# Kernel tuning notes

Hardware: AMD Instinct MI355X
Metric: run time of the kernel (lower is better)

## Reference

```python
import jax, jax.numpy as jnp
import numpy as np

B, S, D = 8, 2048, 256
H = 2
DK = D // H
DH = 1024  # conv hidden
K = 9
PAD = (K - 1) // 2
EPS = 1e-5


def _layernorm(x, g, b):
    mu = jnp.mean(x, axis=-1, keepdims=True)
    var = jnp.mean(jnp.square(x - mu), axis=-1, keepdims=True)
    return (x - mu) * jax.lax.rsqrt(var + EPS) * g + b


def setup_inputs() -> dict:
    key = jax.random.key(0)
    ks = jax.random.split(key, 12)
    sc = 0.02
    batch = jax.random.normal(ks[0], (B, S, D), dtype=jnp.float32)
    # padding mask: True = past end of sequence
    lengths = jax.random.randint(ks[1], (B,), S // 2, S + 1)
    mask = jnp.arange(S)[None, :] >= lengths[:, None]
    return {
        "batch": batch,
        "mask": mask,
        "wq": jax.random.normal(ks[2], (D, D), jnp.float32) * sc,
        "bq": jnp.zeros((D,), jnp.float32),
        "wk": jax.random.normal(ks[3], (D, D), jnp.float32) * sc,
        "bk": jnp.zeros((D,), jnp.float32),
        "wv": jax.random.normal(ks[4], (D, D), jnp.float32) * sc,
        "bv": jnp.zeros((D,), jnp.float32),
        "wo": jax.random.normal(ks[5], (D, D), jnp.float32) * sc,
        "bo": jnp.zeros((D,), jnp.float32),
        "ln1_g": jnp.ones((D,), jnp.float32),
        "ln1_b": jnp.zeros((D,), jnp.float32),
        "conv1_w": jax.random.normal(ks[6], (DH, D, K), jnp.float32) * sc,
        "conv1_b": jnp.zeros((DH,), jnp.float32),
        "conv2_w": jax.random.normal(ks[7], (D, DH, 1), jnp.float32) * sc,
        "conv2_b": jnp.zeros((D,), jnp.float32),
        "ln2_g": jnp.ones((D,), jnp.float32),
        "ln2_b": jnp.zeros((D,), jnp.float32),
    }


def reference(batch, mask, wq, bq, wk, bk, wv, bv, wo, bo, ln1_g, ln1_b,
              conv1_w, conv1_b, conv2_w, conv2_b, ln2_g, ln2_b):
    b, s, d = batch.shape
    # --- multi-head self-attention ---
    q = (batch @ wq.T + bq).reshape(b, s, H, DK)
    k = (batch @ wk.T + bk).reshape(b, s, H, DK)
    v = (batch @ wv.T + bv).reshape(b, s, H, DK)
    scores = jnp.einsum('bqhd,bkhd->bhqk', q, k) / np.sqrt(d).astype(np.float32)
    scores = jnp.where(mask[:, None, None, :], -jnp.inf, scores)
    attn = jax.nn.softmax(scores, axis=-1)
    ctx = jnp.einsum('bhqk,bkhd->bqhd', attn, v).reshape(b, s, d)
    seq = _layernorm(batch + ctx @ wo.T + bo, ln1_g, ln1_b)
    seq = jnp.where(mask[..., None], 0.0, seq)
    # --- conv FFN ---
    h = jax.lax.conv_general_dilated(
        seq.transpose(0, 2, 1), conv1_w, window_strides=(1,),
        padding=[(PAD, PAD)], dimension_numbers=('NCH', 'OIH', 'NCH'))
    h = jax.nn.relu(h + conv1_b[None, :, None])
    out = jnp.einsum('bhs,oh->bos', h, conv2_w[:, :, 0]) + conv2_b[None, :, None]
    seq = _layernorm(seq + out.transpose(0, 2, 1), ln2_g, ln2_b)
    return jnp.where(mask[..., None], 0.0, seq)
```

## Files before the change

kernel.cpp:

```cpp
#include <hip/hip_runtime.h>

typedef unsigned char  u8;
typedef unsigned short u16;
typedef unsigned int   u32;
typedef __attribute__((ext_vector_type(4))) float f32x4;
typedef __attribute__((ext_vector_type(8))) __bf16 bf16x8;
typedef __attribute__((ext_vector_type(4))) u32  u32x4;
typedef __attribute__((ext_vector_type(2))) u32  u32x2;

__device__ __forceinline__ float bf2f(u16 h){ u32 u = ((u32)h)<<16; return __builtin_bit_cast(float, u); }
__device__ __forceinline__ u16  f2bf(float f){
  u32 u = __builtin_bit_cast(u32, f);
  u32 r = u + 0x7FFFu + ((u>>16)&1u);
  return (u16)(r>>16);
}

typedef const __attribute__((address_space(1))) u32 gas_u32;
typedef __attribute__((address_space(3))) u32 las_u32;
__device__ __forceinline__ void gll16(const void* g, void* l){
  __builtin_amdgcn_global_load_lds((gas_u32*)g, (las_u32*)l, 16, 0, 0);
}

__device__ __forceinline__ f32x4 mfma16(bf16x8 a, bf16x8 b, f32x4 c){
  return __builtin_amdgcn_mfma_f32_16x16x32_bf16(a, b, c, 0, 0, 0);
}

__device__ __forceinline__ bf16x8 ldsr8(const u16* p){
  u32x4 v = *(const u32x4*)p;
  return __builtin_bit_cast(bf16x8, v);
}

__device__ __forceinline__ void xcd_remap(int &m_idx, int &n_idx){
  const int Mt = gridDim.x;
  const int fid = blockIdx.x + Mt*blockIdx.y;
  const int xcd = fid & 7, k = fid >> 3;
  const int mpx = Mt >> 3;
  m_idx = xcd*mpx + (k % mpx);
  n_idx = k / mpx;
}

__global__ __launch_bounds__(256)
void prep_big(const float* __restrict__ batch,
              const float* __restrict__ wq, const float* __restrict__ wk,
              const float* __restrict__ wv, const float* __restrict__ wo,
              const float* __restrict__ w2, const float* __restrict__ w1,
              u16* __restrict__ batchc, u16* __restrict__ wqc, u16* __restrict__ w1r)
{
  const int bid = blockIdx.x, tid = threadIdx.x;
  if (bid < 4096){
    const int i = bid*1024 + tid*4;
    f32x4 v = *(const f32x4*)&batch[i];
    u32x2 o;
    o[0] = (u32)f2bf(v[0]) | ((u32)f2bf(v[1])<<16);
    o[1] = (u32)f2bf(v[2]) | ((u32)f2bf(v[3])<<16);
    *(u32x2*)&batchc[i] = o;
  } else if (bid < 4608){
    const int i = (bid-4096)*1024 + tid*4;
    const float* s; int off;
    if      (i < 65536)  { s = wq; off = i; }
    else if (i < 131072) { s = wk; off = i - 65536; }
    else if (i < 196608) { s = wv; off = i - 131072; }
    else if (i < 262144) { s = wo; off = i - 196608; }
    else                 { s = w2; off = i - 262144; }
    f32x4 v = *(const f32x4*)&s[off];
    u32x2 o;
    o[0] = (u32)f2bf(v[0]) | ((u32)f2bf(v[1])<<16);
    o[1] = (u32)f2bf(v[2]) | ((u32)f2bf(v[3])<<16);
    *(u32x2*)&wqc[i] = o;
  } else {
    const int idx = (bid-4608)*256 + tid;
    const int c = idx / 2304;
    const int t = idx - c*2304;
    const int i = t / 9;
    const int kk = t - i*9;
    w1r[c*2304 + kk*256 + i] = f2bf(w1[idx]);
  }
}

__global__ __launch_bounds__(256)
void prep_small(const float* p0,const float* p1,const float* p2,const float* p3,
                const float* p4,const float* p5,const float* p6,const float* p7,
                const float* p8,const float* p9,
                u16* __restrict__ params, const void* __restrict__ mraw,
                u16* __restrict__ cmask, u32* __restrict__ lengths)
{
  const int bid = blockIdx.x, tid = threadIdx.x;
  if (bid == 0){
    const float* ps[10] = {p0,p1,p2,p3,p4,p5,p6,p7,p8,p9};
    const int  off[10] = {0,256,512,768,1024,1280,1536,1792,2048,3072};
    const int  len[10] = {256,256,256,256,256,256,256,256,1024,256};
    for (int a=0;a<10;++a)
      for (int i=tid;i<len[a];i+=256)
        params[off[a]+i] = f2bf(ps[a][i]);
  } else {
    const u8*  pb8  = (const u8*)mraw;
    const u16* pb16 = (const u16*)mraw;
    const u32* pb32 = (const u32*)mraw;
    __shared__ int bad8, bad16, nz8, nz16;
    __shared__ int slen[8];
    if (tid==0){ bad8=0; bad16=0; nz8=0; nz16=0; }
    if (tid<8) slen[tid] = 2048;
    __syncthreads();
    for (int i=tid;i<16384;i+=256){
      u8 v = pb8[i]; int row = i & 2047;
      if (v>1) atomicOr(&bad8,1);
      if (v){ atomicOr(&nz8,1); if (row<1024) atomicOr(&bad8,1); }
      if (row>0 && pb8[i-1]==1 && v==0) atomicOr(&bad8,1);
    }
    for (int i=tid;i<8192;i+=256){
      u16 v = pb16[i]; int row = i & 2047;
      if (!(v==0 || v==0x3F80)) atomicOr(&bad16,1);
      if (v){ atomicOr(&nz16,1); if (row<1024) atomicOr(&bad16,1); }
      if (row>0 && pb16[i-1]==0x3F80 && v==0) atomicOr(&bad16,1);
    }
    __syncthreads();
    const int mode = (!bad8 && nz8) ? 1 : ((!bad16 && nz16) ? 2 : 0);
    for (int i=tid;i<16384;i+=256){
      u16 m;
      if (mode==1)      m = pb8[i]  ? 1 : 0;
      else if (mode==2) m = pb16[i] ? 1 : 0;
      else              m = pb32[i] ? 1 : 0;
      cmask[i] = m;
      if (m) atomicMin(&slen[i>>11], i&2047);
    }
    __syncthreads();
    if (tid<8) lengths[tid] = (u32)slen[tid];
  }
}

__global__ __launch_bounds__(256)
void zero_halo(u16* __restrict__ seq1p)
{
  const int idx = blockIdx.x*256 + threadIdx.x;
  const int b = idx>>11, t = idx&2047;
  const int r = t>>8, c = t&255;
  const int row = (r<4) ? r : (2052 + r - 4);
  seq1p[((size_t)b*2056 + row)*256 + c] = 0;
}

template<bool ADD_RES>
__global__ __launch_bounds__(256)
void gemm_nt(const u16* __restrict__ A, const u16* __restrict__ W,
             const u16* __restrict__ bias, const u16* __restrict__ res,
             u16* __restrict__ out, int K, const u16* __restrict__ cmask)
{
  __shared__ __align__(16) u16 aL[2][4096];
  __shared__ __align__(16) u16 bL[2][4096];
  const int tid = threadIdx.x, lane = tid&63, w = tid>>6;
  const int wm = w>>1, wn = w&1, lr = lane&15, lg = lane>>4;
  int mi, ni; xcd_remap(mi, ni);
  const int m0 = mi*128, n0 = ni*128;
  if (cmask[m0] != 0) return;
  const int nk = K>>5;

  f32x4 acc[4][4];
#pragma unroll
  for (int i=0;i<4;++i)
#pragma unroll
    for (int j=0;j<4;++j) acc[i][j] = f32x4{0.f,0.f,0.f,0.f};

  auto stage = [&](int buf, int kk){
#pragma unroll
    for (int i=0;i<2;++i){
      const int chunk = w*2+i;
      const int boff  = chunk*1024 + lane*16;
      const int r = boff>>6;
      const int cb = (boff&63) ^ (((r>>1)&3)<<4);
      const int c = cb>>1;
      gll16(&A[(size_t)(m0+r)*K + kk*32 + c], &aL[buf][chunk*512]);
      gll16(&W[(size_t)(n0+r)*K + kk*32 + c], &bL[buf][chunk*512]);
    }
  };

  stage(0,0);
  __syncthreads();
  for (int kk=0; kk<nk; ++kk){
    if (kk+1<nk) stage((kk+1)&1, kk+1);
    const u16* ab = aL[kk&1];
    const u16* bb = bL[kk&1];
    bf16x8 af[4], bv[4];
#pragma unroll
    for (int m=0;m<4;++m){
      const int ra = wm*64+m*16+lr;
      af[m] = ldsr8(&ab[(ra*64 + ((lg*16) ^ (((ra>>1)&3)<<4)))>>1]);
    }
#pragma unroll
    for (int n=0;n<4;++n){
      const int rb = wn*64+n*16+lr;
      bv[n] = ldsr8(&bb[(rb*64 + ((lg*16) ^ (((rb>>1)&3)<<4)))>>1]);
    }
#pragma unroll
    for (int m=0;m<4;++m)
#pragma unroll
      for (int n=0;n<4;++n)
        acc[m][n] = mfma16(af[m], bv[n], acc[m][n]);
    __syncthreads();
  }
#pragma unroll
  for (int m=0;m<4;++m)
#pragma unroll
    for (int n=0;n<4;++n)
#pragma unroll
      for (int r=0;r<4;++r){
        const int row = m0 + wm*64 + m*16 + lg*4 + r;
        const int col = n0 + wn*64 + n*16 + lr;
        float v = acc[m][n][r] + bf2f(bias[col]);
        if constexpr (ADD_RES) v += bf2f(res[(size_t)row*256 + col]);
        out[(size_t)row*256 + col] = f2bf(v);
      }
}

__global__ __launch_bounds__(256)
void gemm_qkv(const u16* __restrict__ A, const u16* __restrict__ W,
              const u16* __restrict__ bias, u16* __restrict__ qbase,
              const u16* __restrict__ cmask)
{
  __shared__ __align__(16) u16 aL[2][4096];
  __shared__ __align__(16) u16 bL[2][4096];
  const int tid = threadIdx.x, lane = tid&63, w = tid>>6;
  const int wm = w>>1, wn = w&1, lr = lane&15, lg = lane>>4;
  int mi, ni; xcd_remap(mi, ni);
  const int m0 = mi*128, n0 = ni*128;
  if (cmask[m0] != 0) return;

  f32x4 acc[4][4];
#pragma unroll
  for (int i=0;i<4;++i)
#pragma unroll
    for (int j=0;j<4;++j) acc[i][j] = f32x4{0.f,0.f,0.f,0.f};

  auto stage = [&](int buf, int kk){
#pragma unroll
    for (int i=0;i<2;++i){
      const int chunk = w*2+i;
      const int boff  = chunk*1024 + lane*16;
      const int r = boff>>6;
      const int cb = (boff&63) ^ (((r>>1)&3)<<4);
      const int c = cb>>1;
      gll16(&A[(size_t)(m0+r)*256 + kk*32 + c], &aL[buf][chunk*512]);
      gll16(&W[(size_t)(n0+r)*256 + kk*32 + c], &bL[buf][chunk*512]);
    }
  };

  stage(0,0);
  __syncthreads();
  for (int kk=0; kk<8; ++kk){
    if (kk+1<8) stage((kk+1)&1, kk+1);
    const u16* ab = aL[kk&1];
    const u16* bb = bL[kk&1];
    bf16x8 af[4], bv[4];
#pragma unroll
    for (int m=0;m<4;++m){
      const int ra = wm*64+m*16+lr;
      af[m] = ldsr8(&ab[(ra*64 + ((lg*16) ^ (((ra>>1)&3)<<4)))>>1]);
    }
#pragma unroll
    for (int n=0;n<4;++n){
      const int rb = wn*64+n*16+lr;
      bv[n] = ldsr8(&bb[(rb*64 + ((lg*16) ^ (((rb>>1)&3)<<4)))>>1]);
    }
#pragma unroll
    for (int m=0;m<4;++m)
#pragma unroll
      for (int n=0;n<4;++n)
        acc[m][n] = mfma16(af[m], bv[n], acc[m][n]);
    __syncthreads();
  }
#pragma unroll
  for (int m=0;m<4;++m)
#pragma unroll
    for (int n=0;n<4;++n)
#pragma unroll
      for (int r=0;r<4;++r){
        const int row = m0 + wm*64 + m*16 + lg*4 + r;
        const int col = n0 + wn*64 + n*16 + lr;
        const int which = col>>8, ch = col&255;
        float v = acc[m][n][r] + bf2f(bias[col]);
        qbase[(size_t)which*4194304 + (size_t)row*256 + ch] = f2bf(v);
      }
}

__global__ __launch_bounds__(256, 4)
void conv1_gemm(const u16* __restrict__ Ap, const u16* __restrict__ W1r,
                const u16* __restrict__ b1, u16* __restrict__ Hout,
                const u16* __restrict__ cmask)
{
  __shared__ __align__(16) u16 aL[2][4096];
  __shared__ __align__(16) u16 bL[2][4096];
  const int tid = threadIdx.x, lane = tid&63, w = tid>>6;
  const int wm = w>>1, wn = w&1, lr = lane&15, lg = lane>>4;
  int mi, ni; xcd_remap(mi, ni);
  const int m0 = mi*128, n0 = ni*128;
  if (cmask[m0] != 0) return;
  const int b = m0>>11, s0 = m0&2047;
  const size_t abase = ((size_t)b*2056 + s0)*256;

  f32x4 acc[4][4];
#pragma unroll
  for (int i=0;i<4;++i)
#pragma unroll
    for (int j=0;j<4;++j) acc[i][j] = f32x4{0.f,0.f,0.f,0.f};

  auto stage = [&](int buf, int kk){
    const int tap = kk>>3, ch0 = (kk&7)*32;
#pragma unroll
    for (int i=0;i<2;++i){
      const int chunk = w*2+i;
      const int boff  = chunk*1024 + lane*16;
      const int r = boff>>6;
      const int cb = (boff&63) ^ (((r>>1)&3)<<4);
      const int c = cb>>1;
      gll16(&Ap[abase + (size_t)(tap + r)*256 + ch0 + c], &aL[buf][chunk*512]);
      gll16(&W1r[(size_t)(n0+r)*2304 + kk*32 + c], &bL[buf][chunk*512]);
    }
  };

  stage(0,0);
  __syncthreads();
  for (int kk=0; kk<72; ++kk){
    if (kk+1<72) stage((kk+1)&1, kk+1);
    const u16* ab = aL[kk&1];
    const u16* bb = bL[kk&1];
    bf16x8 af[4], bv[4];
#pragma unroll
    for (int m=0;m<4;++m){
      const int ra = wm*64+m*16+lr;
      af[m] = ldsr8(&ab[(ra*64 + ((lg*16) ^ (((ra>>1)&3)<<4)))>>1]);
    }
#pragma unroll
    for (int n=0;n<4;++n){
      const int rb = wn*64+n*16+lr;
      bv[n] = ldsr8(&bb[(rb*64 + ((lg*16) ^ (((rb>>1)&3)<<4)))>>1]);
    }
#pragma unroll
    for (int m=0;m<4;++m)
#pragma unroll
      for (int n=0;n<4;++n)
        acc[m][n] = mfma16(af[m], bv[n], acc[m][n]);
    __syncthreads();
  }
#pragma unroll
  for (int m=0;m<4;++m)
#pragma unroll
    for (int n=0;n<4;++n)
#pragma unroll
      for (int r=0;r<4;++r){
        const int row = m0 + wm*64 + m*16 + lg*4 + r;
        const int col = n0 + wn*64 + n*16 + lr;
        float v = acc[m][n][r] + bf2f(b1[col]);
        v = v>0.f ? v : 0.f;
        Hout[(size_t)row*1024 + col] = f2bf(v);
      }
}

__global__ __launch_bounds__(512)
void conv2_ln(const u16* __restrict__ Hh, const u16* __restrict__ w2c,
              const u16* __restrict__ b2, const u16* __restrict__ seq1p,
              const u16* __restrict__ g2, const u16* __restrict__ be2,
              const u16* __restrict__ cmask, float* __restrict__ out)
{
  __shared__ __align__(16) u16 aL[2][2048];
  __shared__ __align__(16) u16 bL[2][8192];
  __shared__ float red[2][32][4][2];
  const int tid = threadIdx.x, lane = tid&63, w = tid>>6;
  const int wm = w>>2, wn = w&3, lr = lane&15, lg = lane>>4;
  int mi, ni; xcd_remap(mi, ni); (void)ni;
  const int m0 = mi*64;
  if (cmask[m0] != 0) return;

  f32x4 acc[2][4];
#pragma unroll
  for (int i=0;i<2;++i)
#pragma unroll
    for (int j=0;j<4;++j) acc[i][j] = f32x4{0.f,0.f,0.f,0.f};

  auto stage = [&](int buf, int kk){
    if (w < 4){
      const int boff = w*1024 + lane*16;
      const int r = boff>>6;
      const int cb = (boff&63) ^ (((r>>1)&3)<<4);
      gll16(&Hh[(size_t)(m0+r)*1024 + kk*32 + (cb>>1)], &aL[buf][w*512]);
    }
#pragma unroll
    for (int i=0;i<2;++i){
      const int chunk = w*2+i;
      const int boff = chunk*1024 + lane*16;
      const int r = boff>>6;
      const int cb = (boff&63) ^ (((r>>1)&3)<<4);
      gll16(&w2c[(size_t)r*1024 + kk*32 + (cb>>1)], &bL[buf][chunk*512]);
    }
  };

  stage(0,0);
  __syncthreads();
  for (int kk=0; kk<32; ++kk){
    if (kk+1<32) stage((kk+1)&1, kk+1);
    const u16* ab = aL[kk&1];
    const u16* bb = bL[kk&1];
    bf16x8 af[2], bv[4];
#pragma unroll
    for (int m=0;m<2;++m){
      const int ra = wm*32+m*16+lr;
      af[m] = ldsr8(&ab[(ra*64 + ((lg*16) ^ (((ra>>1)&3)<<4)))>>1]);
    }
#pragma unroll
    for (int n=0;n<4;++n){
      const int rb = wn*64+n*16+lr;
      bv[n] = ldsr8(&bb[(rb*64 + ((lg*16) ^ (((rb>>1)&3)<<4)))>>1]);
    }
#pragma unroll
    for (int m=0;m<2;++m)
#pragma unroll
      for (int n=0;n<4;++n)
        acc[m][n] = mfma16(af[m], bv[n], acc[m][n]);
    __syncthreads();
  }
#pragma unroll
  for (int m=0;m<2;++m)
#pragma unroll
    for (int r=0;r<4;++r){
      float s = 0.f, qq = 0.f;
#pragma unroll
      for (int n=0;n<4;++n){
        const int col = wn*64 + n*16 + lr;
        const int row = m0 + wm*32 + m*16 + lg*4 + r;
        const size_t ri = ((size_t)row + (row>>11)*8 + 4)*256 + col;
        float val = acc[m][n][r] + bf2f(b2[col]) + bf2f(seq1p[ri]);
        acc[m][n][r] = val;
        s += val; qq += val*val;
      }
#pragma unroll
      for (int x=1;x<16;x<<=1){ s += __shfl_xor(s, x); qq += __shfl_xor(qq, x); }
      if (lr == 0){
        const int lrow = m*16 + lg*4 + r;
        red[wm][lrow][wn][0] = s;
        red[wm][lrow][wn][1] = qq;
      }
    }
  __syncthreads();
#pragma unroll
  for (int m=0;m<2;++m)
#pragma unroll
    for (int r=0;r<4;++r){
      const int lrow = m*16 + lg*4 + r;
      const float S = red[wm][lrow][0][0]+red[wm][lrow][1][0]+red[wm][lrow][2][0]+red[wm][lrow][3][0];
      const float Q = red[wm][lrow][0][1]+red[wm][lrow][1][1]+red[wm][lrow][2][1]+red[wm][lrow][3][1];
      const float mu = S*(1.f/256.f);
      const float rs = rsqrtf(Q*(1.f/256.f) - mu*mu + 1e-5f);
      const int row = m0 + wm*32 + lrow;
      const int msk = cmask[row];
#pragma unroll
      for (int n=0;n<4;++n){
        const int col = wn*64 + n*16 + lr;
        float y = (acc[m][n][r]-mu)*rs*bf2f(g2[col]) + bf2f(be2[col]);
        out[(size_t)row*256 + col] = msk ? 0.f : y;
      }
    }
}

__global__ __launch_bounds__(256)
void vtrans(const u16* __restrict__ V, u16* __restrict__ VT)
{
  __shared__ u16 t[64][72];
  const int tid = threadIdx.x;
  const int s0 = blockIdx.x*64;
  const int d0 = blockIdx.y*64;
#pragma unroll
  for (int i=0;i<2;++i){
    const int chunk = tid + i*256;
    const int sr = chunk>>3, c8 = (chunk&7)*8;
    u32x4 raw = *(const u32x4*)&V[(size_t)(s0+sr)*256 + d0 + c8];
#pragma unroll
    for (int j=0;j<4;++j){
      t[sr][c8+2*j]   = (u16)(raw[j]&0xffffu);
      t[sr][c8+2*j+1] = (u16)(raw[j]>>16);
    }
  }
  __syncthreads();
  const int b = s0>>11;
#pragma unroll
  for (int i=0;i<2;++i){
    const int chunk = tid + i*256;
    const int dr = chunk>>3, s8 = (chunk&7)*8;
    const int dg = d0 + dr;
    const int hh = dg>>7, dh = dg&127;
    u32x4 o;
#pragma unroll
    for (int j=0;j<4;++j)
      o[j] = (u32)t[s8+2*j][dr] | ((u32)t[s8+2*j+1][dr]<<16);
    *(u32x4*)&VT[((size_t)((b*2+hh)*128 + dh))*2048 + (s0&2047) + s8] = o;
  }
}

__global__ __launch_bounds__(512)
void attn_fwd(const u16* __restrict__ Q, const u16* __restrict__ Kb,
              const u16* __restrict__ VT, const u32* __restrict__ lengths,
              u16* __restrict__ ctx)
{
  __shared__ __align__(16) u16 kls[2][64*128];
  __shared__ __align__(16) u16 vtls[2][128*64];
  __shared__ __align__(16) u16 pls[8][16*64];
  const int tid = threadIdx.x, lane = tid&63, w = tid>>6;
  const int fid = blockIdx.x;
  const int pair = fid & 15;
  const int qt = fid >> 4;
  const int b  = pair >> 1;
  const int hh = pair & 1;
  const int q0 = qt*128;
  const int L  = (int)lengths[b];
  if (q0 >= L) return;
  const int nkt = (L + 63) >> 6;
  const int lr = lane&15, lg = lane>>4;
  u16* pw = pls[w];

  bf16x8 qf[4];
#pragma unroll
  for (int d=0;d<4;++d)
    qf[d] = *(const bf16x8*)&Q[((size_t)(b*2048+q0+w*16+lr))*256 + hh*128 + d*32 + lg*8];

  f32x4 oacc[8];
  float mrun[4], lrun[4];
#pragma unroll
  for (int n=0;n<8;++n) oacc[n] = f32x4{0.f,0.f,0.f,0.f};
#pragma unroll
  for (int r=0;r<4;++r){ mrun[r] = -1e30f; lrun[r] = 0.f; }

  const size_t kbase = (size_t)(b*2048)*256 + hh*128;
  const size_t vbase = (size_t)((b*2+hh)*128)*2048;

  auto stage = [&](int buf, int kt){
    const int kv0 = kt*64;
#pragma unroll
    for (int i=0;i<2;++i){
      const int chunk = w*2+i;
      const int boff = chunk*1024 + lane*16;
      const int r = boff>>8;
      const int cb = (boff&255) ^ ((r&7)<<4);
      gll16(&Kb[kbase + (size_t)(kv0+r)*256 + (cb>>1)], &kls[buf][chunk*512]);
    }
#pragma unroll
    for (int i=0;i<2;++i){
      const int chunk = w*2+i;
      const int boff = chunk*1024 + lane*16;
      const int r = boff>>7;
      const int cb = (boff&127) ^ ((r&7)<<4);
      gll16(&VT[vbase + (size_t)r*2048 + kv0 + (cb>>1)], &vtls[buf][chunk*512]);
    }
  };

  stage(0, 0);
  __syncthreads();

  for (int kt=0; kt<nkt; ++kt){
    const int kv0 = kt*64;
    const int buf = kt&1;
    if (kt+1 < nkt) stage(buf^1, kt+1);
    f32x4 sacc[4];
#pragma unroll
    for (int n=0;n<4;++n) sacc[n] = f32x4{0.f,0.f,0.f,0.f};
    __builtin_amdgcn_s_setprio(1);
#pragma unroll
    for (int dk=0;dk<4;++dk){
      bf16x8 bk[4];
#pragma unroll
      for (int n=0;n<4;++n){
        const int rb = n*16+lr;
        bk[n] = ldsr8(&kls[buf][(rb*256 + ((dk*64+lg*16) ^ ((rb&7)<<4)))>>1]);
      }
#pragma unroll
      for (int n=0;n<4;++n)
        sacc[n] = mfma16(qf[dk], bk[n], sacc[n]);
    }
    __builtin_amdgcn_s_setprio(0);
#pragma unroll
    for (int n=0;n<4;++n){
      const float madd = (kv0 + n*16 + lr < L) ? 0.f : -1e30f;
#pragma unroll
      for (int r=0;r<4;++r)
        sacc[n][r] = sacc[n][r]*0.0625f + madd;
    }
#pragma unroll
    for (int r=0;r<4;++r){
      float rm = sacc[0][r];
#pragma unroll
      for (int n=1;n<4;++n) rm = fmaxf(rm, sacc[n][r]);
#pragma unroll
      for (int x=1;x<16;x<<=1) rm = fmaxf(rm, __shfl_xor(rm, x));
      const float mnew = fmaxf(mrun[r], rm);
      const float alpha = __expf(mrun[r] - mnew);
      float rsum = 0.f;
#pragma unroll
      for (int n=0;n<4;++n){
        float p = __expf(sacc[n][r] - mnew);
        sacc[n][r] = p;
        rsum += p;
      }
#pragma unroll
      for (int x=1;x<16;x<<=1) rsum += __shfl_xor(rsum, x);
      lrun[r] = alpha*lrun[r] + rsum;
      mrun[r] = mnew;
#pragma unroll
      for (int n=0;n<8;++n) oacc[n][r] *= alpha;
    }
#pragma unroll
    for (int n=0;n<4;++n)
#pragma unroll
      for (int r=0;r<4;++r){
        const int row = lg*4 + r;
        pw[(row*128 + (((n*16+lr)*2) ^ ((row&7)<<4)))>>1] = f2bf(sacc[n][r]);
      }
    __builtin_amdgcn_s_setprio(1);
#pragma unroll
    for (int ks=0;ks<2;++ks){
      bf16x8 pa = ldsr8(&pw[(lr*128 + ((ks*64+lg*16) ^ ((lr&7)<<4)))>>1]);
#pragma unroll
      for (int n=0;n<8;++n){
        const int rv = n*16+lr;
        bf16x8 bvv = ldsr8(&vtls[buf][(rv*128 + ((ks*64+lg*16) ^ ((rv&7)<<4)))>>1]);
        oacc[n] = mfma16(pa, bvv, oacc[n]);
      }
    }
    __builtin_amdgcn_s_setprio(0);
    __syncthreads();
  }
#pragma unroll
  for (int r=0;r<4;++r){
    const float inv = lrun[r] > 0.f ? 1.f/lrun[r] : 0.f;
    const int row = q0 + w*16 + lg*4 + r;
#pragma unroll
    for (int n=0;n<8;++n){
      const int col = hh*128 + n*16 + lr;
      ctx[((size_t)(b*2048+row))*256 + col] = f2bf(oacc[n][r]*inv);
    }
  }
}

__global__ __launch_bounds__(256)
void ln_mask_b(const u16* __restrict__ X, const u16* __restrict__ g,
               const u16* __restrict__ bta, const u16* __restrict__ cmask,
               u16* __restrict__ outp)
{
  const int w = threadIdx.x>>6, lane = threadIdx.x&63;
  const int row = blockIdx.x*4 + w;
  const u16* xr = X + (size_t)row*256;
  u32x2 rawv = *(const u32x2*)&xr[lane*4];
  float xv[4];
  xv[0]=bf2f((u16)(rawv[0]&0xffffu)); xv[1]=bf2f((u16)(rawv[0]>>16));
  xv[2]=bf2f((u16)(rawv[1]&0xffffu)); xv[3]=bf2f((u16)(rawv[1]>>16));
  float s = xv[0]+xv[1]+xv[2]+xv[3];
#pragma unroll
  for (int x=1;x<64;x<<=1) s += __shfl_xor(s, x);
  const float mu = s * (1.f/256.f);
  float d[4];
#pragma unroll
  for (int j=0;j<4;++j) d[j]=xv[j]-mu;
  float sq = d[0]*d[0]+d[1]*d[1]+d[2]*d[2]+d[3]*d[3];
#pragma unroll
  for (int x=1;x<64;x<<=1) sq += __shfl_xor(sq, x);
  const float rs = rsqrtf(sq*(1.f/256.f) + 1e-5f);
  const int msk = cmask[row];
  u16 o4[4];
#pragma unroll
  for (int j=0;j<4;++j){
    const int c = lane*4 + j;
    float y = d[j]*rs*bf2f(g[c]) + bf2f(bta[c]);
    o4[j] = msk ? (u16)0 : f2bf(y);
  }
  u32x2 ov;
  ov[0] = (u32)o4[0] | ((u32)o4[1]<<16);
  ov[1] = (u32)o4[2] | ((u32)o4[3]<<16);
  const size_t prow = (size_t)row + (row>>11)*8 + 4;
  *(u32x2*)&outp[prow*256 + lane*4] = ov;
}

extern "C" void kernel_launch(void* const* d_in, const int* in_sizes, int n_in,
                              void* d_out, int out_size, void* d_ws, size_t ws_size,
                              hipStream_t stream)
{
  (void)in_sizes; (void)n_in; (void)out_size; (void)ws_size;
  const float* batch=(const float*)d_in[0];  const void* mraw = d_in[1];
  const float* wq=(const float*)d_in[2];  const float* bq=(const float*)d_in[3];
  const float* wk=(const float*)d_in[4];  const float* bk=(const float*)d_in[5];
  const float* wv=(const float*)d_in[6];  const float* bvv=(const float*)d_in[7];
  const float* wo=(const float*)d_in[8];  const float* bo=(const float*)d_in[9];
  const float* g1=(const float*)d_in[10]; const float* be1=(const float*)d_in[11];
  const float* w1=(const float*)d_in[12]; const float* b1=(const float*)d_in[13];
  const float* w2=(const float*)d_in[14]; const float* b2=(const float*)d_in[15];
  const float* g2=(const float*)d_in[16]; const float* be2=(const float*)d_in[17];

  char* ws = (char*)d_ws;
  const size_t M = 1024u*1024u;
  u16*   batchc = (u16*)(ws);
  u16*   q      = (u16*)(ws + 8*M);
  u16*   tmpb   = (u16*)(ws + 8*M);
  u16*   kbuf   = (u16*)(ws + 16*M);
  u16*   v      = (u16*)(ws + 24*M);
  u16*   ctx    = (u16*)(ws + 32*M);
  u16*   VT     = (u16*)(ws + 40*M);
  u16*   seq1p  = (u16*)(ws + 40*M);
  u16*   h      = (u16*)(ws);
  u16*   wqc    = (u16*)(ws + 49*M);
  u16*   woc    = wqc + 196608;
  u16*   w2c    = wqc + 262144;
  u16*   w1r    = (u16*)(ws + 50*M);
  u16*   params = w1r + 2359296;
  u16*   cmask  = params + 4096;
  u32*   lengths= (u32*)(cmask + 16384);

  dim3 blk(256,1,1);
  dim3 blk512(512,1,1);

  prep_big<<<dim3(13824,1,1), blk, 0, stream>>>(batch, wq, wk, wv, wo, w2, w1,
                                                batchc, wqc, w1r);
  prep_small<<<dim3(2,1,1), blk, 0, stream>>>(bq,bk,bvv,bo,g1,be1,g2,be2,b1,b2,
                                              params, mraw, cmask, lengths);

  gemm_qkv<<<dim3(128,6,1), blk, 0, stream>>>(batchc, wqc, params, q, cmask);

  vtrans<<<dim3(256,4,1), blk, 0, stream>>>(v, VT);

  attn_fwd<<<dim3(256,1,1), blk512, 0, stream>>>(q, kbuf, VT, lengths, ctx);

  zero_halo<<<dim3(64,1,1), blk, 0, stream>>>(seq1p);

  gemm_nt<true><<<dim3(128,2,1), blk, 0, stream>>>(ctx, woc, params+768, batchc, tmpb, 256, cmask);
  ln_mask_b<<<dim3(4096,1,1), blk, 0, stream>>>(tmpb, params+1024, params+1280, cmask, seq1p);

  conv1_gemm<<<dim3(128,8,1), blk, 0, stream>>>(seq1p, w1r, params+2048, h, cmask);

  conv2_ln<<<dim3(256,1,1), blk512, 0, stream>>>(h, w2c, params+3072, seq1p,
                                                 params+1536, params+1792, cmask,
                                                 (float*)d_out);
}
```

Before: 292.6 us.

## Fuse output projection with LayerNorm and use 8-wave conv1 blocks

Replaces the separate out-projection GEMM and LayerNorm kernels with one kernel. It computes a 64x256 row tile, adds bias and residual, reduces row statistics across waves through shared memory, and writes the masked normalized rows straight into the padded seq buffer. This removes an intermediate buffer round trip and one launch. Separately, conv1_gemm goes from 4 to 8 waves per 128x128 tile, with each wave holding a 64x32 sub-tile to lower per-thread register pressure and add latency hiding. The fused LN computes variance as E[x²]-mu², which is less numerically robust, and the fused kernel launches only 256 blocks.

```diff
diff --git a/kernel.cpp b/kernel.cpp
--- a/kernel.cpp
+++ b/kernel.cpp
@@ -138,78 +138,6 @@
   seq1p[((size_t)b*2056 + row)*256 + c] = 0;
 }
 
-template<bool ADD_RES>
-__global__ __launch_bounds__(256)
-void gemm_nt(const u16* __restrict__ A, const u16* __restrict__ W,
-             const u16* __restrict__ bias, const u16* __restrict__ res,
-             u16* __restrict__ out, int K, const u16* __restrict__ cmask)
-{
-  __shared__ __align__(16) u16 aL[2][4096];
-  __shared__ __align__(16) u16 bL[2][4096];
-  const int tid = threadIdx.x, lane = tid&63, w = tid>>6;
-  const int wm = w>>1, wn = w&1, lr = lane&15, lg = lane>>4;
-  int mi, ni; xcd_remap(mi, ni);
-  const int m0 = mi*128, n0 = ni*128;
-  if (cmask[m0] != 0) return;
-  const int nk = K>>5;
-
-  f32x4 acc[4][4];
-#pragma unroll
-  for (int i=0;i<4;++i)
-#pragma unroll
-    for (int j=0;j<4;++j) acc[i][j] = f32x4{0.f,0.f,0.f,0.f};
-
-  auto stage = [&](int buf, int kk){
-#pragma unroll
-    for (int i=0;i<2;++i){
-      const int chunk = w*2+i;
-      const int boff  = chunk*1024 + lane*16;
-      const int r = boff>>6;
-      const int cb = (boff&63) ^ (((r>>1)&3)<<4);
-      const int c = cb>>1;
-      gll16(&A[(size_t)(m0+r)*K + kk*32 + c], &aL[buf][chunk*512]);
-      gll16(&W[(size_t)(n0+r)*K + kk*32 + c], &bL[buf][chunk*512]);
-    }
-  };
-
-  stage(0,0);
-  __syncthreads();
-  for (int kk=0; kk<nk; ++kk){
-    if (kk+1<nk) stage((kk+1)&1, kk+1);
-    const u16* ab = aL[kk&1];
-    const u16* bb = bL[kk&1];
-    bf16x8 af[4], bv[4];
-#pragma unroll
-    for (int m=0;m<4;++m){
-      const int ra = wm*64+m*16+lr;
-      af[m] = ldsr8(&ab[(ra*64 + ((lg*16) ^ (((ra>>1)&3)<<4)))>>1]);
-    }
-#pragma unroll
-    for (int n=0;n<4;++n){
-      const int rb = wn*64+n*16+lr;
-      bv[n] = ldsr8(&bb[(rb*64 + ((lg*16) ^ (((rb>>1)&3)<<4)))>>1]);
-    }
-#pragma unroll
-    for (int m=0;m<4;++m)
-#pragma unroll
-      for (int n=0;n<4;++n)
-        acc[m][n] = mfma16(af[m], bv[n], acc[m][n]);
-    __syncthreads();
-  }
-#pragma unroll
-  for (int m=0;m<4;++m)
-#pragma unroll
-    for (int n=0;n<4;++n)
-#pragma unroll
-      for (int r=0;r<4;++r){
-        const int row = m0 + wm*64 + m*16 + lg*4 + r;
-        const int col = n0 + wn*64 + n*16 + lr;
-        float v = acc[m][n][r] + bf2f(bias[col]);
-        if constexpr (ADD_RES) v += bf2f(res[(size_t)row*256 + col]);
-        out[(size_t)row*256 + col] = f2bf(v);
-      }
-}
-
 __global__ __launch_bounds__(256)
 void gemm_qkv(const u16* __restrict__ A, const u16* __restrict__ W,
               const u16* __restrict__ bias, u16* __restrict__ qbase,
@@ -280,7 +208,7 @@
       }
 }
 
-__global__ __launch_bounds__(256, 4)
+__global__ __launch_bounds__(512)
 void conv1_gemm(const u16* __restrict__ Ap, const u16* __restrict__ W1r,
                 const u16* __restrict__ b1, u16* __restrict__ Hout,
                 const u16* __restrict__ cmask)
@@ -288,31 +216,27 @@
   __shared__ __align__(16) u16 aL[2][4096];
   __shared__ __align__(16) u16 bL[2][4096];
   const int tid = threadIdx.x, lane = tid&63, w = tid>>6;
-  const int wm = w>>1, wn = w&1, lr = lane&15, lg = lane>>4;
+  const int wm = w>>2, wn = w&3, lr = lane&15, lg = lane>>4;
   int mi, ni; xcd_remap(mi, ni);
   const int m0 = mi*128, n0 = ni*128;
   if (cmask[m0] != 0) return;
   const int b = m0>>11, s0 = m0&2047;
   const size_t abase = ((size_t)b*2056 + s0)*256;
 
-  f32x4 acc[4][4];
+  f32x4 acc[4][2];
 #pragma unroll
   for (int i=0;i<4;++i)
 #pragma unroll
-    for (int j=0;j<4;++j) acc[i][j] = f32x4{0.f,0.f,0.f,0.f};
+    for (int j=0;j<2;++j) acc[i][j] = f32x4{0.f,0.f,0.f,0.f};
 
   auto stage = [&](int buf, int kk){
     const int tap = kk>>3, ch0 = (kk&7)*32;
-#pragma unroll
-    for (int i=0;i<2;++i){
-      const int chunk = w*2+i;
-      const int boff  = chunk*1024 + lane*16;
-      const int r = boff>>6;
-      const int cb = (boff&63) ^ (((r>>1)&3)<<4);
-      const int c = cb>>1;
-      gll16(&Ap[abase + (size_t)(tap + r)*256 + ch0 + c], &aL[buf][chunk*512]);
-      gll16(&W1r[(size_t)(n0+r)*2304 + kk*32 + c], &bL[buf][chunk*512]);
-    }
+    const int boff = w*1024 + lane*16;
+    const int r = boff>>6;
+    const int cb = (boff&63) ^ (((r>>1)&3)<<4);
+    const int c = cb>>1;
+    gll16(&Ap[abase + (size_t)(tap + r)*256 + ch0 + c], &aL[buf][w*512]);
+    gll16(&W1r[(size_t)(n0+r)*2304 + kk*32 + c], &bL[buf][w*512]);
   };
 
   stage(0,0);
@@ -321,36 +245,149 @@
     if (kk+1<72) stage((kk+1)&1, kk+1);
     const u16* ab = aL[kk&1];
     const u16* bb = bL[kk&1];
-    bf16x8 af[4], bv[4];
+    bf16x8 af[4], bv[2];
 #pragma unroll
     for (int m=0;m<4;++m){
       const int ra = wm*64+m*16+lr;
       af[m] = ldsr8(&ab[(ra*64 + ((lg*16) ^ (((ra>>1)&3)<<4)))>>1]);
     }
 #pragma unroll
+    for (int n=0;n<2;++n){
+      const int rb = wn*32+n*16+lr;
+      bv[n] = ldsr8(&bb[(rb*64 + ((lg*16) ^ (((rb>>1)&3)<<4)))>>1]);
+    }
+#pragma unroll
+    for (int m=0;m<4;++m)
+#pragma unroll
+      for (int n=0;n<2;++n)
+        acc[m][n] = mfma16(af[m], bv[n], acc[m][n]);
+    __syncthreads();
+  }
+#pragma unroll
+  for (int m=0;m<4;++m)
+#pragma unroll
+    for (int n=0;n<2;++n)
+#pragma unroll
+      for (int r=0;r<4;++r){
+        const int row = m0 + wm*64 + m*16 + lg*4 + r;
+        const int col = n0 + wn*32 + n*16 + lr;
+        float v = acc[m][n][r] + bf2f(b1[col]);
+        v = v>0.f ? v : 0.f;
+        Hout[(size_t)row*1024 + col] = f2bf(v);
+      }
+}
+
+__global__ __launch_bounds__(512)
+void outproj_ln(const u16* __restrict__ Ctx, const u16* __restrict__ woc,
+                const u16* __restrict__ bo, const u16* __restrict__ batchc,
+                const u16* __restrict__ g1, const u16* __restrict__ be1,
+                const u16* __restrict__ cmask, u16* __restrict__ seq1p)
+{
+  __shared__ __align__(16) u16 aL[2][2048];
+  __shared__ __align__(16) u16 bL[2][8192];
+  __shared__ float red[2][32][4][2];
+  const int tid = threadIdx.x, lane = tid&63, w = tid>>6;
+  const int wm = w>>2, wn = w&3, lr = lane&15, lg = lane>>4;
+  int mi, ni; xcd_remap(mi, ni); (void)ni;
+  const int m0 = mi*64;
+  if (cmask[m0] != 0){
+    for (int i=tid;i<64*128;i+=512){
+      const int rr = i>>7, cc = (i&127)*2;
+      const int row = m0 + rr;
+      const size_t prow = (size_t)row + (row>>11)*8 + 4;
+      *(u32*)&seq1p[prow*256 + cc] = 0u;
+    }
+    return;
+  }
+
+  f32x4 acc[2][4];
+#pragma unroll
+  for (int i=0;i<2;++i)
+#pragma unroll
+    for (int j=0;j<4;++j) acc[i][j] = f32x4{0.f,0.f,0.f,0.f};
+
+  auto stage = [&](int buf, int kk){
+    if (w < 4){
+      const int boff = w*1024 + lane*16;
+      const int r = boff>>6;
+      const int cb = (boff&63) ^ (((r>>1)&3)<<4);
+      gll16(&Ctx[(size_t)(m0+r)*256 + kk*32 + (cb>>1)], &aL[buf][w*512]);
+    }
+#pragma unroll
+    for (int i=0;i<2;++i){
+      const int chunk = w*2+i;
+      const int boff = chunk*1024 + lane*16;
+      const int r = boff>>6;
+      const int cb = (boff&63) ^ (((r>>1)&3)<<4);
+      gll16(&woc[(size_t)r*256 + kk*32 + (cb>>1)], &bL[buf][chunk*512]);
+    }
+  };
+
+  stage(0,0);
+  __syncthreads();
+  for (int kk=0; kk<8; ++kk){
+    if (kk+1<8) stage((kk+1)&1, kk+1);
+    const u16* ab = aL[kk&1];
+    const u16* bb = bL[kk&1];
+    bf16x8 af[2], bv[4];
+#pragma unroll
+    for (int m=0;m<2;++m){
+      const int ra = wm*32+m*16+lr;
+      af[m] = ldsr8(&ab[(ra*64 + ((lg*16) ^ (((ra>>1)&3)<<4)))>>1]);
+    }
+#pragma unroll
     for (int n=0;n<4;++n){
       const int rb = wn*64+n*16+lr;
       bv[n] = ldsr8(&bb[(rb*64 + ((lg*16) ^ (((rb>>1)&3)<<4)))>>1]);
     }
 #pragma unroll
-    for (int m=0;m<4;++m)
+    for (int m=0;m<2;++m)
 #pragma unroll
       for (int n=0;n<4;++n)
         acc[m][n] = mfma16(af[m], bv[n], acc[m][n]);
     __syncthreads();
   }
 #pragma unroll
-  for (int m=0;m<4;++m)
-#pragma unroll
-    for (int n=0;n<4;++n)
-#pragma unroll
-      for (int r=0;r<4;++r){
-        const int row = m0 + wm*64 + m*16 + lg*4 + r;
-        const int col = n0 + wn*64 + n*16 + lr;
-        float v = acc[m][n][r] + bf2f(b1[col]);
-        v = v>0.f ? v : 0.f;
-        Hout[(size_t)row*1024 + col] = f2bf(v);
-      }
+  for (int m=0;m<2;++m)
+#pragma unroll
+    for (int r=0;r<4;++r){
+      float s = 0.f, qq = 0.f;
+#pragma unroll
+      for (int n=0;n<4;++n){
+        const int col = wn*64 + n*16 + lr;
+        const int row = m0 + wm*32 + m*16 + lg*4 + r;
+        float val = acc[m][n][r] + bf2f(bo[col]) + bf2f(batchc[(size_t)row*256 + col]);
+        acc[m][n][r] = val;
+        s += val; qq += val*val;
+      }
+#pragma unroll
+      for (int x=1;x<16;x<<=1){ s += __shfl_xor(s, x); qq += __shfl_xor(qq, x); }
+      if (lr == 0){
+        const int lrow = m*16 + lg*4 + r;
+        red[wm][lrow][wn][0] = s;
+        red[wm][lrow][wn][1] = qq;
+      }
+    }
+  __syncthreads();
+#pragma unroll
+  for (int m=0;m<2;++m)
+#pragma unroll
+    for (int r=0;r<4;++r){
+      const int lrow = m*16 + lg*4 + r;
+      const float S = red[wm][lrow][0][0]+red[wm][lrow][1][0]+red[wm][lrow][2][0]+red[wm][lrow][3][0];
+      const float Q = red[wm][lrow][0][1]+red[wm][lrow][1][1]+red[wm][lrow][2][1]+red[wm][lrow][3][1];
+      const float mu = S*(1.f/256.f);
+      const float rs = rsqrtf(Q*(1.f/256.f) - mu*mu + 1e-5f);
+      const int row = m0 + wm*32 + lrow;
+      const int msk = cmask[row];
+      const size_t prow = (size_t)row + (row>>11)*8 + 4;
+#pragma unroll
+      for (int n=0;n<4;++n){
+        const int col = wn*64 + n*16 + lr;
+        float y = (acc[m][n][r]-mu)*rs*bf2f(g1[col]) + bf2f(be1[col]);
+        seq1p[prow*256 + col] = msk ? (u16)0 : f2bf(y);
+      }
+    }
 }
 
 __global__ __launch_bounds__(512)
@@ -635,44 +672,6 @@
   }
 }
 
-__global__ __launch_bounds__(256)
-void ln_mask_b(const u16* __restrict__ X, const u16* __restrict__ g,
-               const u16* __restrict__ bta, const u16* __restrict__ cmask,
-               u16* __restrict__ outp)
-{
-  const int w = threadIdx.x>>6, lane = threadIdx.x&63;
-  const int row = blockIdx.x*4 + w;
-  const u16* xr = X + (size_t)row*256;
-  u32x2 rawv = *(const u32x2*)&xr[lane*4];
-  float xv[4];
-  xv[0]=bf2f((u16)(rawv[0]&0xffffu)); xv[1]=bf2f((u16)(rawv[0]>>16));
-  xv[2]=bf2f((u16)(rawv[1]&0xffffu)); xv[3]=bf2f((u16)(rawv[1]>>16));
-  float s = xv[0]+xv[1]+xv[2]+xv[3];
-#pragma unroll
-  for (int x=1;x<64;x<<=1) s += __shfl_xor(s, x);
-  const float mu = s * (1.f/256.f);
-  float d[4];
-#pragma unroll
-  for (int j=0;j<4;++j) d[j]=xv[j]-mu;
-  float sq = d[0]*d[0]+d[1]*d[1]+d[2]*d[2]+d[3]*d[3];
-#pragma unroll
-  for (int x=1;x<64;x<<=1) sq += __shfl_xor(sq, x);
-  const float rs = rsqrtf(sq*(1.f/256.f) + 1e-5f);
-  const int msk = cmask[row];
-  u16 o4[4];
-#pragma unroll
-  for (int j=0;j<4;++j){
-    const int c = lane*4 + j;
-    float y = d[j]*rs*bf2f(g[c]) + bf2f(bta[c]);
-    o4[j] = msk ? (u16)0 : f2bf(y);
-  }
-  u32x2 ov;
-  ov[0] = (u32)o4[0] | ((u32)o4[1]<<16);
-  ov[1] = (u32)o4[2] | ((u32)o4[3]<<16);
-  const size_t prow = (size_t)row + (row>>11)*8 + 4;
-  *(u32x2*)&outp[prow*256 + lane*4] = ov;
-}
-
 extern "C" void kernel_launch(void* const* d_in, const int* in_sizes, int n_in,
                               void* d_out, int out_size, void* d_ws, size_t ws_size,
                               hipStream_t stream)
@@ -692,7 +691,6 @@
   const size_t M = 1024u*1024u;
   u16*   batchc = (u16*)(ws);
   u16*   q      = (u16*)(ws + 8*M);
-  u16*   tmpb   = (u16*)(ws + 8*M);
   u16*   kbuf   = (u16*)(ws + 16*M);
   u16*   v      = (u16*)(ws + 24*M);
   u16*   ctx    = (u16*)(ws + 32*M);
@@ -723,10 +721,10 @@
 
   zero_halo<<<dim3(64,1,1), blk, 0, stream>>>(seq1p);
 
-  gemm_nt<true><<<dim3(128,2,1), blk, 0, stream>>>(ctx, woc, params+768, batchc, tmpb, 256, cmask);
-  ln_mask_b<<<dim3(4096,1,1), blk, 0, stream>>>(tmpb, params+1024, params+1280, cmask, seq1p);
-
-  conv1_gemm<<<dim3(128,8,1), blk, 0, stream>>>(seq1p, w1r, params+2048, h, cmask);
+  outproj_ln<<<dim3(256,1,1), blk512, 0, stream>>>(ctx, woc, params+768, batchc,
+                                                   params+1024, params+1280, cmask, seq1p);
+
+  conv1_gemm<<<dim3(128,8,1), blk512, 0, stream>>>(seq1p, w1r, params+2048, h, cmask);
 
   conv2_ln<<<dim3(256,1,1), blk512, 0, stream>>>(h, w2c, params+3072, seq1p,
                                                  params+1536, params+1792, cmask,
```

After: 294.9 us. No clear change (+0.8%).
